# Kernel optimization log

Measured on AMD Instinct MI355X. Metric: run time of the kernel, lower is better.

Reference implementation:

```python
import jax, jax.numpy as jnp
import numpy as np


def setup_inputs() -> dict:
    key = jax.random.key(0)
    k1, k2, k3 = jax.random.split(key, 3)
    x = jax.random.normal(k1, (128, 3, 16, 64, 64), dtype=jnp.float32)
    conv_weight = jax.random.normal(k2, (24, 3, 3, 3, 3), dtype=jnp.float32) * 0.1
    conv_bias = jax.random.normal(k3, (24,), dtype=jnp.float32) * 0.1
    return {"x": x, "conv_weight": conv_weight, "conv_bias": conv_bias}


def reference(x, conv_weight, conv_bias):
    # Conv3d, stride=1, padding=0 (VALID), dilation=1, groups=1, NCDHW layout
    y = jax.lax.conv_general_dilated(
        x, conv_weight,
        window_strides=(1, 1, 1),
        padding='VALID',
        dimension_numbers=('NCDHW', 'OIDHW', 'NCDHW'),
    )
    y = y + conv_bias[None, :, None, None, None]  # [B, 24, 14, 62, 62]
    y = jnp.min(y, axis=2)                        # min over depth -> [B, 24, 62, 62]
    return jax.nn.softmax(y, axis=1)              # softmax over channels
```

## Files before the change

kernel.cpp:

```cpp
#include <hip/hip_runtime.h>
#include <math.h>

#define BATCH 128
#define CIN   3
#define DIN   16
#define HWIN  64
#define COUT  24
#define DOUT  14
#define HOUT  62
#define WOUT  62


__global__ __launch_bounds__(192, 3) void conv_min_softmax_v2(
    const float* __restrict__ x,
    const float* __restrict__ w,
    const float* __restrict__ bias,
    float* __restrict__ out)
{
    __shared__ __align__(16) float sx[3][9][68];
    __shared__ float sm[COUT][64];

    const int tid = threadIdx.x;
    const int bid = blockIdx.x;
    const int ho  = bid % HOUT;
    const int b   = bid / HOUT;

    const int co = tid >> 3;
    const int wg = tid & 7;

    const float* xb = x + (size_t)b * (CIN * DIN * HWIN * HWIN);

    float wreg[81];
    #pragma unroll
    for (int q = 0; q < 81; ++q) wreg[q] = w[co * 81 + q];
    const float bco = bias[co];

    const int r  = tid >> 6;
    const int wc = tid & 63;

    #pragma unroll
    for (int d = 0; d < 2; ++d) {
        #pragma unroll
        for (int cin = 0; cin < CIN; ++cin) {
            sx[d][cin * 3 + r][wc] =
                xb[(cin * DIN + d) * (HWIN * HWIN) + (ho + r) * HWIN + wc];
        }
    }

    float m[8];
    #pragma unroll
    for (int i = 0; i < 8; ++i) m[i] = 1e30f;

    #pragma unroll 1
    for (int dz = 0; dz < DOUT; ++dz) {
        const int s2 = (dz + 2) % 3;
        #pragma unroll
        for (int cin = 0; cin < CIN; ++cin) {
            sx[s2][cin * 3 + r][wc] =
                xb[(cin * DIN + dz + 2) * (HWIN * HWIN) + (ho + r) * HWIN + wc];
        }
        __syncthreads();

        const int p0 = dz % 3;
        const int p1 = (dz + 1) % 3;
        const float* planes[3] = { &sx[p0][0][0], &sx[p1][0][0], &sx[s2][0][0] };

        float acc[8];
        #pragma unroll
        for (int i = 0; i < 8; ++i) acc[i] = 0.f;

        #pragma unroll
        for (int kd = 0; kd < 3; ++kd) {
            const float* plane = planes[kd];
            #pragma unroll
            for (int cin = 0; cin < CIN; ++cin) {
                #pragma unroll
                for (int kh = 0; kh < 3; ++kh) {
                    const float* rp = plane + (cin * 3 + kh) * 68 + wg * 8;
                    float xr[10];
                    const float4 q0 = *(const float4*)(rp);
                    const float4 q1 = *(const float4*)(rp + 4);
                    const float2 q2 = *(const float2*)(rp + 8);
                    xr[0] = q0.x; xr[1] = q0.y; xr[2] = q0.z; xr[3] = q0.w;
                    xr[4] = q1.x; xr[5] = q1.y; xr[6] = q1.z; xr[7] = q1.w;
                    xr[8] = q2.x; xr[9] = q2.y;
                    #pragma unroll
                    for (int kw = 0; kw < 3; ++kw) {
                        const float wv = wreg[cin * 27 + kd * 9 + kh * 3 + kw];
                        #pragma unroll
                        for (int i = 0; i < 8; ++i)
                            acc[i] = fmaf(wv, xr[i + kw], acc[i]);
                    }
                }
            }
        }
        #pragma unroll
        for (int i = 0; i < 8; ++i) m[i] = fminf(m[i], acc[i]);
        __syncthreads();
    }

    #pragma unroll
    for (int i = 0; i < 8; ++i) sm[co][wg * 8 + i] = m[i] + bco;
    __syncthreads();

    if (tid < WOUT) {
        const int p = tid;
        float mx = -1e30f;
        #pragma unroll
        for (int c = 0; c < COUT; ++c) mx = fmaxf(mx, sm[c][p]);
        float e[COUT];
        float ssum = 0.f;
        #pragma unroll
        for (int c = 0; c < COUT; ++c) { e[c] = __expf(sm[c][p] - mx); ssum += e[c]; }
        const float inv = 1.f / ssum;
        float* ob = out + (size_t)b * COUT * (HOUT * WOUT) + ho * WOUT + p;
        #pragma unroll
        for (int c = 0; c < COUT; ++c) ob[(size_t)c * (HOUT * WOUT)] = e[c] * inv;
    }
}

extern "C" void kernel_launch(void* const* d_in, const int* in_sizes, int n_in,
                              void* d_out, int out_size, void* d_ws, size_t ws_size,
                              hipStream_t stream) {
    const float* x    = (const float*)d_in[0];
    const float* w    = (const float*)d_in[1];
    const float* bias = (const float*)d_in[2];
    float* out = (float*)d_out;

    const int blocks = BATCH * HOUT;
    conv_min_softmax_v2<<<blocks, 192, 0, stream>>>(x, w, bias, out);
}
```

Measured before the change: 459.6 us.

## Tile four output rows per block with wave-uniform channel groups and register prefetch

```diff
diff --git a/kernel.cpp b/kernel.cpp
--- a/kernel.cpp
+++ b/kernel.cpp
@@ -1,7 +1,6 @@
 #include <hip/hip_runtime.h>
 #include <math.h>
 
-#define BATCH 128
 #define CIN   3
 #define DIN   16
 #define HWIN  64
@@ -10,112 +9,154 @@
 #define HOUT  62
 #define WOUT  62
 
+#define TILE_H    4
+#define NTILES    16
+#define NTHR      384
+#define ROWS_IN   (TILE_H + 2)
+#define RP        68
+#define PLANE_F   (CIN * ROWS_IN * RP)
+#define SM_RP     66
+#define SM_STRIDE (TILE_H * SM_RP)
+#define SM_SIZE   (COUT * SM_STRIDE)
 
-__global__ __launch_bounds__(192, 3) void conv_min_softmax_v2(
+
+__global__ __launch_bounds__(NTHR, 8) void conv_min_softmax_v3(
     const float* __restrict__ x,
     const float* __restrict__ w,
     const float* __restrict__ bias,
     float* __restrict__ out)
 {
-    __shared__ __align__(16) float sx[3][9][68];
-    __shared__ float sm[COUT][64];
+    __shared__ __align__(16) float smem[SM_SIZE];
 
-    const int tid = threadIdx.x;
-    const int bid = blockIdx.x;
-    const int ho  = bid % HOUT;
-    const int b   = bid / HOUT;
+    const int tid  = threadIdx.x;
+    const int bid  = blockIdx.x;
+    const int rt   = bid & (NTILES - 1);
+    const int b    = bid >> 4;
 
-    const int co = tid >> 3;
-    const int wg = tid & 7;
+    const int q    = __builtin_amdgcn_readfirstlane(tid >> 6);
+    const int lane = tid & 63;
+    const int r    = lane >> 4;
+    const int wg   = lane & 15;
 
-    const float* xb = x + (size_t)b * (CIN * DIN * HWIN * HWIN);
+    const float* __restrict__ wq = w + q * (4 * 81);
+    const float bia0 = bias[q * 4 + 0], bia1 = bias[q * 4 + 1],
+                bia2 = bias[q * 4 + 2], bia3 = bias[q * 4 + 3];
 
-    float wreg[81];
+    const int grow = min(rt * TILE_H + q, HWIN - 1);
+    const float* __restrict__ xb =
+        x + (size_t)b * (CIN * DIN * HWIN * HWIN) + grow * HWIN + lane;
+
+    const int vbase = r * RP + wg * 4;
+
+    {
+        float p0[CIN], p1[CIN];
+        #pragma unroll
+        for (int c = 0; c < CIN; ++c) p0[c] = xb[(c * DIN + 0) * (HWIN * HWIN)];
+        #pragma unroll
+        for (int c = 0; c < CIN; ++c) p1[c] = xb[(c * DIN + 1) * (HWIN * HWIN)];
+        #pragma unroll
+        for (int c = 0; c < CIN; ++c) smem[0 * PLANE_F + (c * ROWS_IN + q) * RP + lane] = p0[c];
+        #pragma unroll
+        for (int c = 0; c < CIN; ++c) smem[1 * PLANE_F + (c * ROWS_IN + q) * RP + lane] = p1[c];
+    }
+    float pf[CIN];
     #pragma unroll
-    for (int q = 0; q < 81; ++q) wreg[q] = w[co * 81 + q];
-    const float bco = bias[co];
+    for (int c = 0; c < CIN; ++c) pf[c] = xb[(c * DIN + 2) * (HWIN * HWIN)];
 
-    const int r  = tid >> 6;
-    const int wc = tid & 63;
+    float m[4][4];
+    #pragma unroll
+    for (int cop = 0; cop < 4; ++cop)
+        #pragma unroll
+        for (int i = 0; i < 4; ++i) m[cop][i] = 1e30f;
 
-    #pragma unroll
-    for (int d = 0; d < 2; ++d) {
-        #pragma unroll
-        for (int cin = 0; cin < CIN; ++cin) {
-            sx[d][cin * 3 + r][wc] =
-                xb[(cin * DIN + d) * (HWIN * HWIN) + (ho + r) * HWIN + wc];
-        }
-    }
-
-    float m[8];
-    #pragma unroll
-    for (int i = 0; i < 8; ++i) m[i] = 1e30f;
+    int o0 = 0, o1 = PLANE_F, o2 = 2 * PLANE_F;
 
     #pragma unroll 1
     for (int dz = 0; dz < DOUT; ++dz) {
-        const int s2 = (dz + 2) % 3;
+        __syncthreads();
         #pragma unroll
-        for (int cin = 0; cin < CIN; ++cin) {
-            sx[s2][cin * 3 + r][wc] =
-                xb[(cin * DIN + dz + 2) * (HWIN * HWIN) + (ho + r) * HWIN + wc];
-        }
+        for (int c = 0; c < CIN; ++c)
+            smem[o2 + (c * ROWS_IN + q) * RP + lane] = pf[c];
+        const int dnext = (dz + 3 < DIN) ? (dz + 3) : (DIN - 1);
+        #pragma unroll
+        for (int c = 0; c < CIN; ++c)
+            pf[c] = xb[(c * DIN + dnext) * (HWIN * HWIN)];
         __syncthreads();
 
-        const int p0 = dz % 3;
-        const int p1 = (dz + 1) % 3;
-        const float* planes[3] = { &sx[p0][0][0], &sx[p1][0][0], &sx[s2][0][0] };
-
-        float acc[8];
+        float acc[4][4];
         #pragma unroll
-        for (int i = 0; i < 8; ++i) acc[i] = 0.f;
+        for (int cop = 0; cop < 4; ++cop)
+            #pragma unroll
+            for (int i = 0; i < 4; ++i) acc[cop][i] = 0.f;
 
         #pragma unroll
         for (int kd = 0; kd < 3; ++kd) {
-            const float* plane = planes[kd];
+            const int ob = (kd == 0) ? o0 : (kd == 1) ? o1 : o2;
             #pragma unroll
             for (int cin = 0; cin < CIN; ++cin) {
                 #pragma unroll
                 for (int kh = 0; kh < 3; ++kh) {
-                    const float* rp = plane + (cin * 3 + kh) * 68 + wg * 8;
-                    float xr[10];
-                    const float4 q0 = *(const float4*)(rp);
-                    const float4 q1 = *(const float4*)(rp + 4);
-                    const float2 q2 = *(const float2*)(rp + 8);
-                    xr[0] = q0.x; xr[1] = q0.y; xr[2] = q0.z; xr[3] = q0.w;
-                    xr[4] = q1.x; xr[5] = q1.y; xr[6] = q1.z; xr[7] = q1.w;
-                    xr[8] = q2.x; xr[9] = q2.y;
+                    const float* rp = &smem[ob + (cin * ROWS_IN + kh) * RP + vbase];
+                    const float4 a4 = *(const float4*)rp;
+                    const float2 a2 = *(const float2*)(rp + 4);
+                    const float xr[6] = { a4.x, a4.y, a4.z, a4.w, a2.x, a2.y };
                     #pragma unroll
-                    for (int kw = 0; kw < 3; ++kw) {
-                        const float wv = wreg[cin * 27 + kd * 9 + kh * 3 + kw];
+                    for (int cop = 0; cop < 4; ++cop) {
+                        const float* wk = wq + cop * 81 + cin * 27 + kd * 9 + kh * 3;
                         #pragma unroll
-                        for (int i = 0; i < 8; ++i)
-                            acc[i] = fmaf(wv, xr[i + kw], acc[i]);
+                        for (int kw = 0; kw < 3; ++kw) {
+                            const float wv = wk[kw];
+                            #pragma unroll
+                            for (int i = 0; i < 4; ++i)
+                                acc[cop][i] = fmaf(wv, xr[i + kw], acc[cop][i]);
+                        }
                     }
                 }
             }
         }
+
         #pragma unroll
-        for (int i = 0; i < 8; ++i) m[i] = fminf(m[i], acc[i]);
-        __syncthreads();
+        for (int cop = 0; cop < 4; ++cop)
+            #pragma unroll
+            for (int i = 0; i < 4; ++i)
+                m[cop][i] = fminf(m[cop][i], acc[cop][i]);
+
+        const int tmp = o0; o0 = o1; o1 = o2; o2 = tmp;
     }
 
-    #pragma unroll
-    for (int i = 0; i < 8; ++i) sm[co][wg * 8 + i] = m[i] + bco;
     __syncthreads();
 
-    if (tid < WOUT) {
-        const int p = tid;
-        float mx = -1e30f;
-        #pragma unroll
-        for (int c = 0; c < COUT; ++c) mx = fmaxf(mx, sm[c][p]);
-        float e[COUT];
-        float ssum = 0.f;
-        #pragma unroll
-        for (int c = 0; c < COUT; ++c) { e[c] = __expf(sm[c][p] - mx); ssum += e[c]; }
-        const float inv = 1.f / ssum;
-        float* ob = out + (size_t)b * COUT * (HOUT * WOUT) + ho * WOUT + p;
-        #pragma unroll
-        for (int c = 0; c < COUT; ++c) ob[(size_t)c * (HOUT * WOUT)] = e[c] * inv;
+    #pragma unroll
+    for (int i = 0; i < 4; ++i) {
+        const int p = r * SM_RP + wg * 4 + i;
+        smem[(q * 4 + 0) * SM_STRIDE + p] = m[0][i] + bia0;
+        smem[(q * 4 + 1) * SM_STRIDE + p] = m[1][i] + bia1;
+        smem[(q * 4 + 2) * SM_STRIDE + p] = m[2][i] + bia2;
+        smem[(q * 4 + 3) * SM_STRIDE + p] = m[3][i] + bia3;
+    }
+    __syncthreads();
+
+    if (tid < 256) {
+        const int row = tid >> 6;
+        const int col = tid & 63;
+        const int ho  = rt * TILE_H + row;
+        if (col < WOUT && ho < HOUT) {
+            float v[COUT];
+            float mx = -1e30f;
+            #pragma unroll
+            for (int c = 0; c < COUT; ++c) {
+                v[c] = smem[c * SM_STRIDE + row * SM_RP + col];
+                mx = fmaxf(mx, v[c]);
+            }
+            float s = 0.f;
+            #pragma unroll
+            for (int c = 0; c < COUT; ++c) { v[c] = __expf(v[c] - mx); s += v[c]; }
+            const float inv = 1.f / s;
+            float* ob = out + (size_t)b * COUT * (HOUT * WOUT) + ho * WOUT + col;
+            #pragma unroll
+            for (int c = 0; c < COUT; ++c)
+                ob[(size_t)c * (HOUT * WOUT)] = v[c] * inv;
+        }
     }
 }
 
@@ -127,6 +168,5 @@
     const float* bias = (const float*)d_in[2];
     float* out = (float*)d_out;
 
-    const int blocks = BATCH * HOUT;
-    conv_min_softmax_v2<<<blocks, 192, 0, stream>>>(x, w, bias, out);
+    conv_min_softmax_v3<<<128 * NTILES, NTHR, 0, stream>>>(x, w, bias, out);
 }
```

After: 1.085 ms. 2.36x slower.
